# Performance work log

Hardware: AMD Instinct MI355X
Metric: run time of the kernel (lower is better)

Reference implementation:

```python
import jax, jax.numpy as jnp
import numpy as np

SUBSET_RATE = 0.7


def setup_inputs() -> dict:
    key = jax.random.key(0)
    k1, k2 = jax.random.split(key)
    B, L = 8192, 4096
    x = jax.random.normal(k1, (B, L), dtype=jnp.float32)
    # realistic tail-padding mask: True = padded; valid lengths in [1, L]
    lengths = jax.random.randint(k2, (B,), 1, L + 1)
    mask = jnp.arange(L)[None, :] >= lengths[:, None]  # [B, L] bool
    return {"x": x, "mask": mask}


def reference(x, mask):
    # Non-bool tensors pass through unchanged.
    B, L = mask.shape
    # per-row valid length = (~record).sum()
    lengths = jnp.sum(~mask, axis=-1)  # [B] int32
    # cutoff = min(ceil(length * rate), L - 1)
    cutoff = jnp.minimum(
        jnp.ceil(lengths.astype(jnp.float32) * SUBSET_RATE).astype(jnp.int32),
        L - 1,
    )  # [B]
    # record[cutoff:] = True  (suffix fill), keep existing True bits
    new_mask = mask | (jnp.arange(L, dtype=jnp.int32)[None, :] >= cutoff[:, None])
    return x, new_mask
```

## Files before the change

### kernel.cpp

```cpp
#include <hip/hip_runtime.h>


#define L_DIM 4096
#define SUBSET_RATE 0.7f

typedef float        f32x4 __attribute__((ext_vector_type(4)));
typedef unsigned int u32x4 __attribute__((ext_vector_type(4)));

__global__ void detect_mode_kernel(const unsigned int* __restrict__ m,
                                   int* __restrict__ mode) {
    __shared__ int any_gt1, any_f32;
    if (threadIdx.x == 0) { any_gt1 = 0; any_f32 = 0; }
    __syncthreads();
    int lgt1 = 0, lf32 = 0;
    for (int i = threadIdx.x; i < L_DIM; i += blockDim.x) {
        unsigned int w = m[i];
        if (w == 0x3f800000u)      lf32 = 1;
        else if (w > 1u)           lgt1 = 1;
    }
    if (lgt1) any_gt1 = 1;
    if (lf32) any_f32 = 1;
    __syncthreads();
    if (threadIdx.x == 0)
        *mode = (any_f32 ? 0 : (any_gt1 ? 1 : 0));
}

__global__ __launch_bounds__(256)
void subset_kernel(const float* __restrict__ x,
                   const void* __restrict__ mask,
                   const int* __restrict__ mode_p,
                   float* __restrict__ out_x,
                   float* __restrict__ out_mask) {
    const int row  = blockIdx.x;
    const int t    = threadIdx.x;
    const int mode = *mode_p;
    const size_t rowoff = (size_t)row * L_DIM;

    const f32x4* xr  = (const f32x4*)(x        + rowoff);
    f32x4*       oxr = (f32x4*)      (out_x    + rowoff);
    f32x4*       omr = (f32x4*)      (out_mask + rowoff);

    unsigned int bits = 0;

    if (mode == 1) {
        const unsigned int* mp =
            (const unsigned int*)((const unsigned char*)mask + rowoff);
        unsigned int mw[4];
        #pragma unroll
        for (int k = 0; k < 4; ++k)
            mw[k] = __builtin_nontemporal_load(&mp[t + 256 * k]);
        f32x4 xv[4];
        #pragma unroll
        for (int k = 0; k < 4; ++k)
            xv[k] = __builtin_nontemporal_load(&xr[t + 256 * k]);
        #pragma unroll
        for (int k = 0; k < 4; ++k) {
            #pragma unroll
            for (int j = 0; j < 4; ++j)
                if ((mw[k] >> (8 * j)) & 0xffu) bits |= 1u << (4 * k + j);
        }
        #pragma unroll
        for (int k = 0; k < 4; ++k)
            __builtin_nontemporal_store(xv[k], &oxr[t + 256 * k]);
    } else {
        const u32x4* mp = (const u32x4*)((const unsigned int*)mask + rowoff);
        u32x4 mw[4];
        #pragma unroll
        for (int k = 0; k < 4; ++k)
            mw[k] = __builtin_nontemporal_load(&mp[t + 256 * k]);
        f32x4 xv[4];
        #pragma unroll
        for (int k = 0; k < 4; ++k)
            xv[k] = __builtin_nontemporal_load(&xr[t + 256 * k]);
        #pragma unroll
        for (int k = 0; k < 4; ++k) {
            if (mw[k].x) bits |= 1u << (4 * k + 0);
            if (mw[k].y) bits |= 1u << (4 * k + 1);
            if (mw[k].z) bits |= 1u << (4 * k + 2);
            if (mw[k].w) bits |= 1u << (4 * k + 3);
        }
        #pragma unroll
        for (int k = 0; k < 4; ++k)
            __builtin_nontemporal_store(xv[k], &oxr[t + 256 * k]);
    }

    int zeros = 16 - __popc(bits);

    #pragma unroll
    for (int off = 32; off > 0; off >>= 1)
        zeros += __shfl_down(zeros, off, 64);
    __shared__ int partial[4];
    __shared__ int cutoff_s;
    if ((t & 63) == 0) partial[t >> 6] = zeros;
    __syncthreads();
    if (t == 0) {
        int len = partial[0] + partial[1] + partial[2] + partial[3];
        cutoff_s = min((int)ceilf((float)len * SUBSET_RATE), L_DIM - 1);
    }
    __syncthreads();
    const int cutoff = cutoff_s;

    #pragma unroll
    for (int k = 0; k < 4; ++k) {
        const int c  = t + 256 * k;
        const int i0 = c * 4;
        f32x4 mv;
        mv.x = (((bits >> (4 * k + 0)) & 1u) || (i0 + 0 >= cutoff)) ? 1.0f : 0.0f;
        mv.y = (((bits >> (4 * k + 1)) & 1u) || (i0 + 1 >= cutoff)) ? 1.0f : 0.0f;
        mv.z = (((bits >> (4 * k + 2)) & 1u) || (i0 + 2 >= cutoff)) ? 1.0f : 0.0f;
        mv.w = (((bits >> (4 * k + 3)) & 1u) || (i0 + 3 >= cutoff)) ? 1.0f : 0.0f;
        __builtin_nontemporal_store(mv, &omr[c]);
    }
}

extern "C" void kernel_launch(void* const* d_in, const int* in_sizes, int n_in,
                              void* d_out, int out_size, void* d_ws, size_t ws_size,
                              hipStream_t stream) {
    const float* x    = (const float*)d_in[0];
    const void*  mask = d_in[1];
    const int B = in_sizes[0] / L_DIM;

    float* out_x    = (float*)d_out;
    float* out_mask = out_x + (size_t)B * L_DIM;
    int*   mode     = (int*)d_ws;

    detect_mode_kernel<<<1, 256, 0, stream>>>((const unsigned int*)mask, mode);
    subset_kernel<<<B, 256, 0, stream>>>(x, mask, mode, out_x, out_mask);
}
```

Before: 422.6 us.

## Assign one row per wavefront and reduce with shuffles instead of block barriers

Each 64-lane wavefront now handles a whole row, so a block of 256 threads covers four rows. The row-length reduction becomes a pure xor-shuffle all-reduce, which removes the shared-memory partials and both __syncthreads. The byte-mask path counts nonzero bytes with bit tricks instead of per-byte branches. In exchange each lane holds 16 float4s of x in registers (64 VGPRs plus the mask words), which raises register pressure against the new launch bound of 4.

```diff
diff --git a/kernel.cpp b/kernel.cpp
--- a/kernel.cpp
+++ b/kernel.cpp
@@ -25,14 +25,18 @@
         *mode = (any_f32 ? 0 : (any_gt1 ? 1 : 0));
 }
 
-__global__ __launch_bounds__(256)
+__global__ __launch_bounds__(256, 4)
 void subset_kernel(const float* __restrict__ x,
                    const void* __restrict__ mask,
                    const int* __restrict__ mode_p,
                    float* __restrict__ out_x,
-                   float* __restrict__ out_mask) {
-    const int row  = blockIdx.x;
-    const int t    = threadIdx.x;
+                   float* __restrict__ out_mask,
+                   int B) {
+    const int wave = threadIdx.x >> 6;
+    const int lane = threadIdx.x & 63;
+    const int row  = blockIdx.x * 4 + wave;
+    if (row >= B) return;
+
     const int mode = *mode_p;
     const size_t rowoff = (size_t)row * L_DIM;
 
@@ -40,76 +44,63 @@
     f32x4*       oxr = (f32x4*)      (out_x    + rowoff);
     f32x4*       omr = (f32x4*)      (out_mask + rowoff);
 
-    unsigned int bits = 0;
+    unsigned long long bits = 0ull;
+    f32x4 xv[16];
 
     if (mode == 1) {
         const unsigned int* mp =
             (const unsigned int*)((const unsigned char*)mask + rowoff);
-        unsigned int mw[4];
+        unsigned int mw[16];
         #pragma unroll
-        for (int k = 0; k < 4; ++k)
-            mw[k] = __builtin_nontemporal_load(&mp[t + 256 * k]);
-        f32x4 xv[4];
+        for (int m = 0; m < 16; ++m)
+            mw[m] = __builtin_nontemporal_load(&mp[lane + 64 * m]);
         #pragma unroll
-        for (int k = 0; k < 4; ++k)
-            xv[k] = __builtin_nontemporal_load(&xr[t + 256 * k]);
+        for (int m = 0; m < 16; ++m)
+            xv[m] = __builtin_nontemporal_load(&xr[lane + 64 * m]);
         #pragma unroll
-        for (int k = 0; k < 4; ++k) {
-            #pragma unroll
-            for (int j = 0; j < 4; ++j)
-                if ((mw[k] >> (8 * j)) & 0xffu) bits |= 1u << (4 * k + j);
+        for (int m = 0; m < 16; ++m) {
+            unsigned int w  = mw[m];
+            unsigned int nz = w | (w >> 4);
+            nz |= nz >> 2;
+            nz |= nz >> 1;
+            nz &= 0x01010101u;
+            unsigned int nib = (nz * 0x01020408u) >> 24;
+            bits |= (unsigned long long)(nib & 0xFu) << (4 * m);
         }
-        #pragma unroll
-        for (int k = 0; k < 4; ++k)
-            __builtin_nontemporal_store(xv[k], &oxr[t + 256 * k]);
     } else {
         const u32x4* mp = (const u32x4*)((const unsigned int*)mask + rowoff);
-        u32x4 mw[4];
         #pragma unroll
-        for (int k = 0; k < 4; ++k)
-            mw[k] = __builtin_nontemporal_load(&mp[t + 256 * k]);
-        f32x4 xv[4];
+        for (int m = 0; m < 16; ++m)
+            xv[m] = __builtin_nontemporal_load(&xr[lane + 64 * m]);
         #pragma unroll
-        for (int k = 0; k < 4; ++k)
-            xv[k] = __builtin_nontemporal_load(&xr[t + 256 * k]);
-        #pragma unroll
-        for (int k = 0; k < 4; ++k) {
-            if (mw[k].x) bits |= 1u << (4 * k + 0);
-            if (mw[k].y) bits |= 1u << (4 * k + 1);
-            if (mw[k].z) bits |= 1u << (4 * k + 2);
-            if (mw[k].w) bits |= 1u << (4 * k + 3);
+        for (int m = 0; m < 16; ++m) {
+            u32x4 w = __builtin_nontemporal_load(&mp[lane + 64 * m]);
+            unsigned int nib = (w.x ? 1u : 0u) | (w.y ? 2u : 0u)
+                             | (w.z ? 4u : 0u) | (w.w ? 8u : 0u);
+            bits |= (unsigned long long)nib << (4 * m);
         }
-        #pragma unroll
-        for (int k = 0; k < 4; ++k)
-            __builtin_nontemporal_store(xv[k], &oxr[t + 256 * k]);
     }
 
-    int zeros = 16 - __popc(bits);
+    int zeros = 64 - __popcll(bits);
+    #pragma unroll
+    for (int off = 1; off < 64; off <<= 1)
+        zeros += __shfl_xor(zeros, off, 64);
+
+    const int cutoff = min((int)ceilf((float)zeros * SUBSET_RATE), L_DIM - 1);
 
     #pragma unroll
-    for (int off = 32; off > 0; off >>= 1)
-        zeros += __shfl_down(zeros, off, 64);
-    __shared__ int partial[4];
-    __shared__ int cutoff_s;
-    if ((t & 63) == 0) partial[t >> 6] = zeros;
-    __syncthreads();
-    if (t == 0) {
-        int len = partial[0] + partial[1] + partial[2] + partial[3];
-        cutoff_s = min((int)ceilf((float)len * SUBSET_RATE), L_DIM - 1);
-    }
-    __syncthreads();
-    const int cutoff = cutoff_s;
+    for (int m = 0; m < 16; ++m)
+        __builtin_nontemporal_store(xv[m], &oxr[lane + 64 * m]);
 
     #pragma unroll
-    for (int k = 0; k < 4; ++k) {
-        const int c  = t + 256 * k;
-        const int i0 = c * 4;
+    for (int m = 0; m < 16; ++m) {
+        const int i0 = 4 * lane + 256 * m;
         f32x4 mv;
-        mv.x = (((bits >> (4 * k + 0)) & 1u) || (i0 + 0 >= cutoff)) ? 1.0f : 0.0f;
-        mv.y = (((bits >> (4 * k + 1)) & 1u) || (i0 + 1 >= cutoff)) ? 1.0f : 0.0f;
-        mv.z = (((bits >> (4 * k + 2)) & 1u) || (i0 + 2 >= cutoff)) ? 1.0f : 0.0f;
-        mv.w = (((bits >> (4 * k + 3)) & 1u) || (i0 + 3 >= cutoff)) ? 1.0f : 0.0f;
-        __builtin_nontemporal_store(mv, &omr[c]);
+        mv.x = (((bits >> (4 * m + 0)) & 1ull) || (i0 + 0 >= cutoff)) ? 1.0f : 0.0f;
+        mv.y = (((bits >> (4 * m + 1)) & 1ull) || (i0 + 1 >= cutoff)) ? 1.0f : 0.0f;
+        mv.z = (((bits >> (4 * m + 2)) & 1ull) || (i0 + 2 >= cutoff)) ? 1.0f : 0.0f;
+        mv.w = (((bits >> (4 * m + 3)) & 1ull) || (i0 + 3 >= cutoff)) ? 1.0f : 0.0f;
+        __builtin_nontemporal_store(mv, &omr[lane + 64 * m]);
     }
 }
 
@@ -125,5 +116,5 @@
     int*   mode     = (int*)d_ws;
 
     detect_mode_kernel<<<1, 256, 0, stream>>>((const unsigned int*)mask, mode);
-    subset_kernel<<<B, 256, 0, stream>>>(x, mask, mode, out_x, out_mask);
+    subset_kernel<<<(B + 3) / 4, 256, 0, stream>>>(x, mask, mode, out_x, out_mask, B);
 }
```

Result: no change. 428.3 us (+1.3%).
